# Kernel optimization log

Measured on AMD Instinct MI355X. Metric: run time of the kernel, lower is better.

Reference implementation:

```python
import jax, jax.numpy as jnp
import numpy as np

WINDOW_SIZE = 11
SIGMA = 1.5
C1 = 0.01 ** 2
C2 = 0.03 ** 2
L1_WEIGHT = 1.0
SSIM_WEIGHT = 1.0


def _gaussian_window(channels, window_size=WINDOW_SIZE, sigma=SIGMA):
    x = np.arange(window_size, dtype=np.float32) - window_size // 2
    g = np.exp(-(x ** 2) / (2.0 * sigma ** 2))
    g = g / g.sum()
    w2d = np.outer(g, g).astype(np.float32)  # [ws, ws]
    # depthwise kernel layout OIHW with I=1, O=channels
    return jnp.asarray(np.tile(w2d[None, None], (channels, 1, 1, 1)))


def _dwconv(x, w):
    pad = WINDOW_SIZE // 2
    return jax.lax.conv_general_dilated(
        x, w, window_strides=(1, 1), padding=[(pad, pad), (pad, pad)],
        dimension_numbers=('NCHW', 'OIHW', 'NCHW'),
        feature_group_count=x.shape[1])


def setup_inputs() -> dict:
    key = jax.random.key(0)
    k1, k2 = jax.random.split(key)
    shape = (16, 3, 512, 512)
    outputs = jax.random.uniform(k1, shape, dtype=jnp.float32)
    labels = jax.random.uniform(k2, shape, dtype=jnp.float32)
    return {"outputs": outputs, "labels": labels}


def reference(outputs, labels):
    img1, img2 = outputs, labels
    channel = img1.shape[1]
    window = _gaussian_window(channel).astype(img1.dtype)

    mu1 = _dwconv(img1, window)
    mu2 = _dwconv(img2, window)
    mu1_sq = mu1 * mu1
    mu2_sq = mu2 * mu2
    mu1_mu2 = mu1 * mu2
    sigma1_sq = _dwconv(img1 * img1, window) - mu1_sq
    sigma2_sq = _dwconv(img2 * img2, window) - mu2_sq
    sigma12 = _dwconv(img1 * img2, window) - mu1_mu2

    ssim_map = ((2 * mu1_mu2 + C1) * (2 * sigma12 + C2)) / (
        (mu1_sq + mu2_sq + C1) * (sigma1_sq + sigma2_sq + C2))
    ssim = jnp.mean(ssim_map)

    l1_loss = jnp.mean(jnp.abs(outputs - labels))
    ssim_loss = 1.0 - ssim
    return L1_WEIGHT * l1_loss + SSIM_WEIGHT * ssim_loss
```

## Files before the change

### kernel.cpp

```cpp
#include <hip/hip_runtime.h>
#include <hip/hip_bf16.h>
#include <math.h>

#define IMG 512
#define TW 64
#define TH 32
#define NTX 8
#define NTY 16
#define NIMG 48
#define NBLOCKS (NTX * NTY * NIMG)
#define NPIX (16LL * 3 * 512 * 512)

#define C1F 0.0001f
#define C2F 0.0009f

#define SR 88
#define TR 56

typedef __attribute__((ext_vector_type(8))) short short8;
typedef __attribute__((ext_vector_type(4))) float float4v;

#define GW0 0.00102838f
#define GW1 0.00759877f
#define GW2 0.03600077f
#define GW3 0.10936069f
#define GW4 0.21300539f
#define GW5 0.26601172f

__device__ __forceinline__ unsigned short f2bf(float f) {
    unsigned u = __builtin_bit_cast(unsigned, f);
    u += 0x7FFF + ((u >> 16) & 1);
    return (unsigned short)(u >> 16);
}
__device__ __forceinline__ unsigned pk2(float a, float b) {
    __hip_bfloat162 h = __float22bfloat162_rn(make_float2(a, b));
    unsigned u;
    __builtin_memcpy(&u, &h, 4);
    return u;
}

__global__ __launch_bounds__(256, 3)
void ssim_tile_kernel(const float* __restrict__ xg, const float* __restrict__ yg,
                      float* __restrict__ partials) {
    __shared__ unsigned short sbuf[2][48][SR];
    __shared__ unsigned short tbuf[5][TW][TR];
    __shared__ unsigned short gwtbl[16];
    __shared__ float red[8];

    const int tid  = threadIdx.x;
    const int lane = tid & 63;
    const int w    = tid >> 6;
    const int q    = lane >> 4;
    const int n16  = lane & 15;

    const int img = blockIdx.z;
    const int r00  = blockIdx.y * TH - 5;
    const int c00a = blockIdx.x * TW - 8;
    const float* __restrict__ xi = xg + (size_t)img * (IMG * IMG);
    const float* __restrict__ yi = yg + (size_t)img * (IMG * IMG);

    if (tid < 16) {
        const float gwf[11] = {GW0, GW1, GW2, GW3, GW4, GW5, GW4, GW3, GW2, GW1, GW0};
        unsigned short v = 0;
        #pragma unroll
        for (int t = 0; t < 11; ++t)
            if (tid == t) v = f2bf(gwf[t]);
        gwtbl[tid] = v;
    }

    for (int u = tid; u < 960; u += 256) {
        int pr  = u / 20;
        int pc4 = (u - pr * 20) << 2;
        int gr = r00 + pr, gc = c00a + pc4;
        float4 xv = make_float4(0.f, 0.f, 0.f, 0.f);
        float4 yv = make_float4(0.f, 0.f, 0.f, 0.f);
        if (pr < 42 && (unsigned)gr < 512u && (unsigned)gc < 512u) {
            size_t o = (size_t)gr * IMG + gc;
            xv = *(const float4*)(xi + o);
            yv = *(const float4*)(yi + o);
        }
        *(uint2*)&sbuf[0][pr][pc4] = make_uint2(pk2(xv.x, xv.y), pk2(xv.z, xv.w));
        *(uint2*)&sbuf[1][pr][pc4] = make_uint2(pk2(yv.x, yv.y), pk2(yv.z, yv.w));
    }

    float l1_loc;
    {
        int r  = tid >> 3;
        int c8 = (tid & 7) << 3;
        size_t o = (size_t)(blockIdx.y * TH + r) * IMG + blockIdx.x * TW + c8;
        float4 a0 = *(const float4*)(xi + o);
        float4 a1 = *(const float4*)(xi + o + 4);
        float4 b0 = *(const float4*)(yi + o);
        float4 b1 = *(const float4*)(yi + o + 4);
        l1_loc = fabsf(a0.x - b0.x) + fabsf(a0.y - b0.y) + fabsf(a0.z - b0.z) + fabsf(a0.w - b0.w)
               + fabsf(a1.x - b1.x) + fabsf(a1.y - b1.y) + fabsf(a1.z - b1.z) + fabsf(a1.w - b1.w);
    }
    __syncthreads();

    short8 bh, bv;
    {
        int baseh = q * 8 - n16 - 3;
        int basev = q * 8 - n16;
        #pragma unroll
        for (int j = 0; j < 8; ++j) {
            unsigned ih = min((unsigned)(baseh + j), 15u);
            unsigned iv = min((unsigned)(basev + j), 15u);
            bh[j] = (short)gwtbl[ih];
            bv[j] = (short)gwtbl[iv];
        }
    }

    #pragma unroll
    for (int i = 0; i < 3; ++i) {
        int u = w + i * 4;
        int rg = u >> 2, cg = u & 3;
        short8 ax = *(const short8*)&sbuf[0][rg * 16 + n16][cg * 16 + q * 8];
        short8 ay = *(const short8*)&sbuf[1][rg * 16 + n16][cg * 16 + q * 8];
        short8 axx, ayy, axy;
        {
            unsigned* px = (unsigned*)&ax;
            unsigned* py = (unsigned*)&ay;
            unsigned* pxx = (unsigned*)&axx;
            unsigned* pyy = (unsigned*)&ayy;
            unsigned* pxy = (unsigned*)&axy;
            #pragma unroll
            for (int r = 0; r < 4; ++r) {
                unsigned rx = px[r], ry = py[r];
                float xlo = __builtin_bit_cast(float, rx << 16);
                float xhi = __builtin_bit_cast(float, rx & 0xFFFF0000u);
                float ylo = __builtin_bit_cast(float, ry << 16);
                float yhi = __builtin_bit_cast(float, ry & 0xFFFF0000u);
                pxx[r] = pk2(xlo * xlo, xhi * xhi);
                pyy[r] = pk2(ylo * ylo, yhi * yhi);
                pxy[r] = pk2(xlo * ylo, xhi * yhi);
            }
        }
        float4v d;
        d = __builtin_amdgcn_mfma_f32_16x16x32_bf16(ax, bh, (float4v){0.f,0.f,0.f,0.f}, 0, 0, 0);
        *(uint2*)&tbuf[0][cg * 16 + n16][rg * 16 + q * 4] = make_uint2(pk2(d[0], d[1]), pk2(d[2], d[3]));
        d = __builtin_amdgcn_mfma_f32_16x16x32_bf16(ay, bh, (float4v){0.f,0.f,0.f,0.f}, 0, 0, 0);
        *(uint2*)&tbuf[1][cg * 16 + n16][rg * 16 + q * 4] = make_uint2(pk2(d[0], d[1]), pk2(d[2], d[3]));
        d = __builtin_amdgcn_mfma_f32_16x16x32_bf16(axx, bh, (float4v){0.f,0.f,0.f,0.f}, 0, 0, 0);
        *(uint2*)&tbuf[2][cg * 16 + n16][rg * 16 + q * 4] = make_uint2(pk2(d[0], d[1]), pk2(d[2], d[3]));
        d = __builtin_amdgcn_mfma_f32_16x16x32_bf16(ayy, bh, (float4v){0.f,0.f,0.f,0.f}, 0, 0, 0);
        *(uint2*)&tbuf[3][cg * 16 + n16][rg * 16 + q * 4] = make_uint2(pk2(d[0], d[1]), pk2(d[2], d[3]));
        d = __builtin_amdgcn_mfma_f32_16x16x32_bf16(axy, bh, (float4v){0.f,0.f,0.f,0.f}, 0, 0, 0);
        *(uint2*)&tbuf[4][cg * 16 + n16][rg * 16 + q * 4] = make_uint2(pk2(d[0], d[1]), pk2(d[2], d[3]));
    }
    __syncthreads();

    float ssim_loc = 0.f;
    #pragma unroll
    for (int rgp = 0; rgp < 2; ++rgp) {
        float4v acc5[5];
        #pragma unroll
        for (int ch = 0; ch < 5; ++ch) {
            short8 a = *(const short8*)&tbuf[ch][w * 16 + n16][rgp * 16 + q * 8];
            acc5[ch] = __builtin_amdgcn_mfma_f32_16x16x32_bf16(
                a, bv, (float4v){0.f, 0.f, 0.f, 0.f}, 0, 0, 0);
        }
        #pragma unroll
        for (int r = 0; r < 4; ++r) {
            float mu1 = acc5[0][r], mu2 = acc5[1][r];
            float e11 = acc5[2][r], e22 = acc5[3][r], e12 = acc5[4][r];
            float m1s = mu1 * mu1, m2s = mu2 * mu2, m12 = mu1 * mu2;
            float v1 = e11 - m1s, v2 = e22 - m2s, v12 = e12 - m12;
            float num = (2.f * m12 + C1F) * (2.f * v12 + C2F);
            float den = (m1s + m2s + C1F) * (v1 + v2 + C2F);
            ssim_loc = fmaf(num, __builtin_amdgcn_rcpf(den), ssim_loc);
        }
    }

    #pragma unroll
    for (int off = 32; off > 0; off >>= 1) {
        ssim_loc += __shfl_down(ssim_loc, off);
        l1_loc   += __shfl_down(l1_loc, off);
    }
    if (lane == 0) {
        red[w] = ssim_loc;
        red[4 + w] = l1_loc;
    }
    __syncthreads();
    if (tid == 0) {
        float ss = red[0] + red[1] + red[2] + red[3];
        float ll = red[4] + red[5] + red[6] + red[7];
        int bid = blockIdx.x + NTX * (blockIdx.y + NTY * blockIdx.z);
        partials[bid] = ss;
        partials[NBLOCKS + bid] = ll;
    }
}

__global__ __launch_bounds__(1024)
void finalize_kernel(const float* __restrict__ partials, float* __restrict__ out) {
    __shared__ double rs[16], rl[16];
    const int tid = threadIdx.x;
    double ss = 0.0, ll = 0.0;
    for (int i = tid; i < NBLOCKS; i += 1024) {
        ss += (double)partials[i];
        ll += (double)partials[NBLOCKS + i];
    }
    #pragma unroll
    for (int off = 32; off > 0; off >>= 1) {
        ss += __shfl_down(ss, off);
        ll += __shfl_down(ll, off);
    }
    int wave = tid >> 6, lane = tid & 63;
    if (lane == 0) { rs[wave] = ss; rl[wave] = ll; }
    __syncthreads();
    if (tid == 0) {
        double sst = 0.0, llt = 0.0;
        #pragma unroll
        for (int w = 0; w < 16; ++w) { sst += rs[w]; llt += rl[w]; }
        double invn = 1.0 / (double)NPIX;
        out[0] = (float)(llt * invn + (1.0 - sst * invn));
    }
}

extern "C" void kernel_launch(void* const* d_in, const int* in_sizes, int n_in,
                              void* d_out, int out_size, void* d_ws, size_t ws_size,
                              hipStream_t stream) {
    const float* x = (const float*)d_in[0];
    const float* y = (const float*)d_in[1];
    float* out = (float*)d_out;
    float* partials = (float*)d_ws;

    dim3 grid(NTX, NTY, NIMG);
    ssim_tile_kernel<<<grid, dim3(256), 0, stream>>>(x, y, partials);
    finalize_kernel<<<1, dim3(1024), 0, stream>>>(partials, out);
}
```

Measured before the change: 157.3 us.

## Keep horizontal-pass results in registers and feed vertical MFMA directly

The horizontal Gaussian pass now assigns each wave one column group and keeps its MFMA outputs, packed to bf16, in registers. The vertical pass consumes them directly as operands of two chained 16x16x16 bf16 MFMAs. This removes the transpose buffer in shared memory, one block barrier, and the LDS write and read round trip. The lower LDS footprint lets launch bounds ask for 5 blocks per CU, at the cost of more live registers per thread.

```diff
diff --git a/kernel.cpp b/kernel.cpp
--- a/kernel.cpp
+++ b/kernel.cpp
@@ -15,10 +15,19 @@
 #define C2F 0.0009f
 
 #define SR 88
-#define TR 56
-
+
+typedef __attribute__((ext_vector_type(4))) short short4v;
 typedef __attribute__((ext_vector_type(8))) short short8;
 typedef __attribute__((ext_vector_type(4))) float float4v;
+typedef __attribute__((ext_vector_type(2))) unsigned uint2v;
+
+__device__ __forceinline__ float4v mfma16(short4v a, short4v b, float4v c) {
+#if defined(__HIP_DEVICE_COMPILE__)
+    return __builtin_amdgcn_mfma_f32_16x16x16bf16_1k(a, b, c, 0, 0, 0);
+#else
+    return c;
+#endif
+}
 
 #define GW0 0.00102838f
 #define GW1 0.00759877f
@@ -39,11 +48,10 @@
     return u;
 }
 
-__global__ __launch_bounds__(256, 3)
+__global__ __launch_bounds__(256, 5)
 void ssim_tile_kernel(const float* __restrict__ xg, const float* __restrict__ yg,
                       float* __restrict__ partials) {
     __shared__ unsigned short sbuf[2][48][SR];
-    __shared__ unsigned short tbuf[5][TW][TR];
     __shared__ unsigned short gwtbl[16];
     __shared__ float red[8];
 
@@ -97,25 +105,27 @@
     }
     __syncthreads();
 
-    short8 bh, bv;
+    short8 bh;
+    short4v bv0, bv1;
     {
         int baseh = q * 8 - n16 - 3;
-        int basev = q * 8 - n16;
-        #pragma unroll
-        for (int j = 0; j < 8; ++j) {
-            unsigned ih = min((unsigned)(baseh + j), 15u);
-            unsigned iv = min((unsigned)(basev + j), 15u);
-            bh[j] = (short)gwtbl[ih];
-            bv[j] = (short)gwtbl[iv];
-        }
-    }
-
-    #pragma unroll
-    for (int i = 0; i < 3; ++i) {
-        int u = w + i * 4;
-        int rg = u >> 2, cg = u & 3;
-        short8 ax = *(const short8*)&sbuf[0][rg * 16 + n16][cg * 16 + q * 8];
-        short8 ay = *(const short8*)&sbuf[1][rg * 16 + n16][cg * 16 + q * 8];
+        #pragma unroll
+        for (int j = 0; j < 8; ++j)
+            bh[j] = (short)gwtbl[min((unsigned)(baseh + j), 15u)];
+        int base0 = q * 4 - n16, base1 = q * 4 + 16 - n16;
+        #pragma unroll
+        for (int j = 0; j < 4; ++j) {
+            bv0[j] = (short)gwtbl[min((unsigned)(base0 + j), 15u)];
+            bv1[j] = (short)gwtbl[min((unsigned)(base1 + j), 15u)];
+        }
+    }
+
+    const float4v zero4 = {0.f, 0.f, 0.f, 0.f};
+    uint2v d1[3][5];
+    #pragma unroll
+    for (int rg = 0; rg < 3; ++rg) {
+        short8 ax = *(const short8*)&sbuf[0][rg * 16 + n16][w * 16 + q * 8];
+        short8 ay = *(const short8*)&sbuf[1][rg * 16 + n16][w * 16 + q * 8];
         short8 axx, ayy, axy;
         {
             unsigned* px = (unsigned*)&ax;
@@ -136,18 +146,17 @@
             }
         }
         float4v d;
-        d = __builtin_amdgcn_mfma_f32_16x16x32_bf16(ax, bh, (float4v){0.f,0.f,0.f,0.f}, 0, 0, 0);
-        *(uint2*)&tbuf[0][cg * 16 + n16][rg * 16 + q * 4] = make_uint2(pk2(d[0], d[1]), pk2(d[2], d[3]));
-        d = __builtin_amdgcn_mfma_f32_16x16x32_bf16(ay, bh, (float4v){0.f,0.f,0.f,0.f}, 0, 0, 0);
-        *(uint2*)&tbuf[1][cg * 16 + n16][rg * 16 + q * 4] = make_uint2(pk2(d[0], d[1]), pk2(d[2], d[3]));
-        d = __builtin_amdgcn_mfma_f32_16x16x32_bf16(axx, bh, (float4v){0.f,0.f,0.f,0.f}, 0, 0, 0);
-        *(uint2*)&tbuf[2][cg * 16 + n16][rg * 16 + q * 4] = make_uint2(pk2(d[0], d[1]), pk2(d[2], d[3]));
-        d = __builtin_amdgcn_mfma_f32_16x16x32_bf16(ayy, bh, (float4v){0.f,0.f,0.f,0.f}, 0, 0, 0);
-        *(uint2*)&tbuf[3][cg * 16 + n16][rg * 16 + q * 4] = make_uint2(pk2(d[0], d[1]), pk2(d[2], d[3]));
-        d = __builtin_amdgcn_mfma_f32_16x16x32_bf16(axy, bh, (float4v){0.f,0.f,0.f,0.f}, 0, 0, 0);
-        *(uint2*)&tbuf[4][cg * 16 + n16][rg * 16 + q * 4] = make_uint2(pk2(d[0], d[1]), pk2(d[2], d[3]));
-    }
-    __syncthreads();
+        d = __builtin_amdgcn_mfma_f32_16x16x32_bf16(ax, bh, zero4, 0, 0, 0);
+        d1[rg][0] = (uint2v){pk2(d[0], d[1]), pk2(d[2], d[3])};
+        d = __builtin_amdgcn_mfma_f32_16x16x32_bf16(ay, bh, zero4, 0, 0, 0);
+        d1[rg][1] = (uint2v){pk2(d[0], d[1]), pk2(d[2], d[3])};
+        d = __builtin_amdgcn_mfma_f32_16x16x32_bf16(axx, bh, zero4, 0, 0, 0);
+        d1[rg][2] = (uint2v){pk2(d[0], d[1]), pk2(d[2], d[3])};
+        d = __builtin_amdgcn_mfma_f32_16x16x32_bf16(ayy, bh, zero4, 0, 0, 0);
+        d1[rg][3] = (uint2v){pk2(d[0], d[1]), pk2(d[2], d[3])};
+        d = __builtin_amdgcn_mfma_f32_16x16x32_bf16(axy, bh, zero4, 0, 0, 0);
+        d1[rg][4] = (uint2v){pk2(d[0], d[1]), pk2(d[2], d[3])};
+    }
 
     float ssim_loc = 0.f;
     #pragma unroll
@@ -155,9 +164,9 @@
         float4v acc5[5];
         #pragma unroll
         for (int ch = 0; ch < 5; ++ch) {
-            short8 a = *(const short8*)&tbuf[ch][w * 16 + n16][rgp * 16 + q * 8];
-            acc5[ch] = __builtin_amdgcn_mfma_f32_16x16x32_bf16(
-                a, bv, (float4v){0.f, 0.f, 0.f, 0.f}, 0, 0, 0);
+            short4v a1 = __builtin_bit_cast(short4v, d1[rgp + 1][ch]);
+            short4v a0 = __builtin_bit_cast(short4v, d1[rgp][ch]);
+            acc5[ch] = mfma16(a0, bv0, mfma16(a1, bv1, zero4));
         }
         #pragma unroll
         for (int r = 0; r < 4; ++r) {
```

After: 145.5 us. -7.5%, faster.
